# Kernel tuning notes

Measured on AMD Instinct MI355X. Metric: run time of the kernel, lower is better.

The kernel has to match this reference:

```python
import jax, jax.numpy as jnp
import numpy as np

B = 128        # graphs
NPG = 64       # nodes per graph (num_node)
N = B * NPG    # total nodes = 8192
IN = 16        # in_channels
D = 128        # d_model
OUT = 64       # out_channels
CAT = IN * NPG + NPG * NPG  # 5120
EPS = 1e-5


def _lin_init(k, fi, fo):
    s = 1.0 / np.sqrt(fi)
    kw, kb = jax.random.split(k)
    W = jax.random.uniform(kw, (fi, fo), jnp.float32, -s, s)
    b = jax.random.uniform(kb, (fo,), jnp.float32, -s, s)
    return W, b


def setup_inputs() -> dict:
    key = jax.random.key(0)
    ks = jax.random.split(key, 10)
    x = jax.random.normal(ks[0], (N, IN), jnp.float32)
    # complete graph (all i->j pairs, incl. self loops) per graph, offset per graph
    ii = np.repeat(np.arange(NPG), NPG)
    jj = np.tile(np.arange(NPG), NPG)
    off = (np.arange(B) * NPG)[:, None]
    row = (ii[None, :] + off).reshape(-1)
    col = (jj[None, :] + off).reshape(-1)
    edge_index = jnp.asarray(np.stack([row, col]), jnp.int32)  # [2, E]
    E = edge_index.shape[1]
    edge_weight = jax.random.uniform(ks[1], (E,), jnp.float32)
    batch = jnp.repeat(jnp.arange(B, dtype=jnp.int32), NPG)
    W1, b1 = _lin_init(ks[2], IN, D)
    W2, b2 = _lin_init(ks[3], D, D)
    Wm0, bm0 = _lin_init(ks[4], D + CAT, D)
    Wm1, bm1 = _lin_init(ks[5], D, D)
    Wm2, bm2 = _lin_init(ks[6], D, D)
    Wout, bout = _lin_init(ks[7], D, OUT)
    ones = jnp.ones((D,), jnp.float32)
    zeros = jnp.zeros((D,), jnp.float32)
    return dict(x=x, edge_index=edge_index, edge_weight=edge_weight, batch=batch,
                W1=W1, b1=b1, W2=W2, b2=b2,
                Wm0=Wm0, bm0=bm0, g0=ones, be0=zeros,
                Wm1=Wm1, bm1=bm1, g1=ones, be1=zeros,
                Wm2=Wm2, bm2=bm2, g2=ones, be2=zeros,
                Wout=Wout, bout=bout)


def _gcn_conv(h_in, row, col, ew, W, b):
    # PyG GCNConv: linear first, then D^-1/2 (A) D^-1/2 aggregation (self loops already present)
    h = h_in @ W                                             # [N, F]
    deg = jax.ops.segment_sum(ew, col, num_segments=N)       # in-degree by edge weight
    dinv = jnp.where(deg > 0, jax.lax.rsqrt(deg), 0.0)
    norm = dinv[row] * ew * dinv[col]                        # [E]
    out = jax.ops.segment_sum(norm[:, None] * h[row], col, num_segments=N)
    return out + b


def _bn(h, g, b):
    # BatchNorm1d, training-mode math (biased variance), eps=1e-5
    m = jnp.mean(h, axis=0)
    v = jnp.var(h, axis=0)
    return g * (h - m) * jax.lax.rsqrt(v + EPS) + b


def reference(x, edge_index, edge_weight, batch,
              W1, b1, W2, b2,
              Wm0, bm0, g0, be0,
              Wm1, bm1, g1, be1,
              Wm2, bm2, g2, be2,
              Wout, bout):
    row, col = edge_index[0], edge_index[1]
    h = _gcn_conv(x, row, col, edge_weight, W1, b1)
    h = jax.nn.relu(h)
    h = _gcn_conv(h, row, col, edge_weight, W2, b2)
    # global_mean_pool
    sums = jax.ops.segment_sum(h, batch, num_segments=B)
    cnt = jax.ops.segment_sum(jnp.ones((N,), h.dtype), batch, num_segments=B)
    pooled = sums / cnt[:, None]
    pooled = jax.nn.relu(pooled)
    feat = jnp.concatenate([pooled, x.reshape(B, -1), edge_weight.reshape(B, -1)], axis=1)
    feat = jax.nn.relu(feat)
    h = _bn(jax.nn.relu(feat @ Wm0 + bm0), g0, be0)
    h = _bn(jax.nn.relu(h @ Wm1 + bm1), g1, be1)
    h = _bn(jax.nn.relu(h @ Wm2 + bm2), g2, be2)
    return h @ Wout + bout
```

## Files before the change

### kernel.cpp

```cpp
#include <hip/hip_runtime.h>

#define NG 128
#define NPG 64
#define IN 16
#define DM 128
#define NOUT 64
#define EPG 4096
#define NCH 128
#define BN_EPS 1e-5f

__global__ __launch_bounds__(512) void k_front(
    const float* __restrict__ x, const float* __restrict__ ew,
    const float* __restrict__ W1, const float* __restrict__ b1,
    const float* __restrict__ W2, const float* __restrict__ b2,
    const float* __restrict__ Wm0,
    float* __restrict__ part, float* __restrict__ ppart,
    float* __restrict__ stats)
{
    __shared__ __align__(16) float u[16128];
    const int bid = blockIdx.x, t = threadIdx.x;

    if (bid < 128) {
        float* ew_s     = u;
        float* x_s      = u + 4096;
        float* W1_s     = u + 5120;
        float* P_s      = u + 7168;
        float* b1_s     = u + 15360;
        float* dinv_s   = u + 15488;
        float* t_s      = u + 15552;
        float* zp       = u + 4096;
        float* z_full   = u + 15616;
        float* pooled_s = u + 15744;
        float* pp4      = u + 4096;
        const int g = bid;
        if (bid == 0) {
            for (int i = t; i < 768; i += 512) stats[i] = 0.f;
        }
        {
            const float4* ew4 = (const float4*)(ew + g * EPG);
            float4* ews4 = (float4*)ew_s;
            ews4[t]       = ew4[t];
            ews4[t + 512] = ew4[t + 512];
            if (t < 256) {
                const int xi = t & 63, k4 = (t >> 6) * 4;
                float4 xv = *(const float4*)(x + g * NPG * IN + xi * IN + k4);
                x_s[(k4 + 0) * 64 + xi] = xv.x;
                x_s[(k4 + 1) * 64 + xi] = xv.y;
                x_s[(k4 + 2) * 64 + xi] = xv.z;
                x_s[(k4 + 3) * 64 + xi] = xv.w;
            }
            ((float4*)W1_s)[t] = ((const float4*)W1)[t];
            if (t < 128) b1_s[t] = b1[t];
        }
        __syncthreads();

        if (t < NPG) {
            float s = 0.f;
            #pragma unroll 8
            for (int i = 0; i < NPG; i++) s += ew_s[i * NPG + t];
            dinv_s[t] = (s > 0.f) ? rsqrtf(s) : 0.f;
        }
        __syncthreads();

        {
            const int j = t & 63, q = t >> 6;
            const float dj = dinv_s[j];
            for (int i = q * 8; i < q * 8 + 8; i++) {
                float vv = ew_s[i * NPG + j] * dj;
                #pragma unroll
                for (int off = 32; off > 0; off >>= 1) vv += __shfl_down(vv, off, 64);
                if (j == 0) t_s[i] = dinv_s[i] * vv * (1.f / 64.f);
            }
        }

        {
            const int it = t & 15, ft = t >> 4;
            const int i0 = it * 4, f0 = ft * 4;
            float accp[4][4];
            #pragma unroll
            for (int a = 0; a < 4; a++)
                #pragma unroll
                for (int c = 0; c < 4; c++) accp[a][c] = 0.f;
            #pragma unroll
            for (int k = 0; k < IN; k++) {
                const float4 a4 = *(const float4*)(x_s + k * 64 + i0);
                const float4 b4 = *(const float4*)(W1_s + k * DM + f0);
                const float av[4] = {a4.x, a4.y, a4.z, a4.w};
                const float bv[4] = {b4.x, b4.y, b4.z, b4.w};
                #pragma unroll
                for (int a = 0; a < 4; a++)
                    #pragma unroll
                    for (int c = 0; c < 4; c++) accp[a][c] += av[a] * bv[c];
            }
            #pragma unroll
            for (int a = 0; a < 4; a++) {
                const float di = dinv_s[i0 + a];
                *(float4*)(P_s + (i0 + a) * DM + f0) =
                    make_float4(di * accp[a][0], di * accp[a][1],
                                di * accp[a][2], di * accp[a][3]);
            }
        }
        __syncthreads();

        {
            const int jt = t & 15, ft = t >> 4;
            const int j0 = jt * 4, f0 = ft * 4;
            float acc[4][4];
            #pragma unroll
            for (int a = 0; a < 4; a++)
                #pragma unroll
                for (int c = 0; c < 4; c++) acc[a][c] = 0.f;
            #pragma unroll 4
            for (int k = 0; k < 64; k++) {
                const float4 a4 = *(const float4*)(ew_s + k * 64 + j0);
                const float4 b4 = *(const float4*)(P_s + k * DM + f0);
                const float av[4] = {a4.x, a4.y, a4.z, a4.w};
                const float bv[4] = {b4.x, b4.y, b4.z, b4.w};
                #pragma unroll
                for (int a = 0; a < 4; a++)
                    #pragma unroll
                    for (int c = 0; c < 4; c++) acc[a][c] += av[a] * bv[c];
            }
            float zpart[4];
            #pragma unroll
            for (int c = 0; c < 4; c++) zpart[c] = 0.f;
            #pragma unroll
            for (int a = 0; a < 4; a++) {
                const float dj = dinv_s[j0 + a], tj = t_s[j0 + a];
                #pragma unroll
                for (int c = 0; c < 4; c++) {
                    float h = fmaxf(dj * acc[a][c] + b1_s[f0 + c], 0.f);
                    zpart[c] += tj * h;
                }
            }
            *(float4*)(zp + jt * 132 + f0) =
                make_float4(zpart[0], zpart[1], zpart[2], zpart[3]);
        }
        __syncthreads();

        if (t < 128) {
            float s = 0.f;
            #pragma unroll
            for (int jt = 0; jt < 16; jt++) s += zp[jt * 132 + t];
            z_full[t] = s;
        }
        __syncthreads();

        {
            const int c = t & 127, kh = t >> 7;
            float acc = 0.f;
            #pragma unroll 8
            for (int k = kh * 32; k < kh * 32 + 32; k++)
                acc += z_full[k] * W2[k * DM + c];
            pp4[kh * 128 + c] = acc;
        }
        __syncthreads();
        if (t < 128)
            pooled_s[t] = fmaxf(pp4[t] + pp4[128 + t] + pp4[256 + t] + pp4[384 + t]
                                + b2[t], 0.f);
        __syncthreads();

        {
            const int f = t & 127, kh = t >> 7;
            float acc = 0.f;
            #pragma unroll 8
            for (int k = kh * 32; k < kh * 32 + 32; k++)
                acc += pooled_s[k] * Wm0[k * DM + f];
            pp4[kh * 128 + f] = acc;
        }
        __syncthreads();
        if (t < 128)
            ppart[g * DM + t] = pp4[t] + pp4[128 + t] + pp4[256 + t] + pp4[384 + t];
    } else {
        const int c = bid - 128;
        const int kc = c >> 1, fh = c & 1;
        const int K0 = kc * 80;
        float* a_s = u;
        float* b_s = u + 10560;

        float4 ra[4], ra2, rb[3];
        #pragma unroll
        for (int it = 0; it < 4; it++) {
            int idx = it * 512 + t;
            int gg = idx >> 4, k4 = (idx & 15) << 2;
            int K = K0 + k4;
            const float* src = (K < 1024) ? (x + gg * 1024 + K)
                                          : (ew + gg * 4096 + (K - 1024));
            ra[it] = *(const float4*)src;
        }
        {
            int gg = t >> 2, k4 = 64 + ((t & 3) << 2);
            int K = K0 + k4;
            const float* src = (K < 1024) ? (x + gg * 1024 + K)
                                          : (ew + gg * 4096 + (K - 1024));
            ra2 = *(const float4*)src;
        }
        #pragma unroll
        for (int it = 0; it < 3; it++) {
            int idx = it * 512 + t;
            if (idx < 1280) {
                int k = idx >> 4, fl4 = (idx & 15) << 2;
                rb[it] = *(const float4*)(Wm0 + (size_t)(128 + K0 + k) * 128
                                          + fh * 64 + fl4);
            }
        }
        #pragma unroll
        for (int it = 0; it < 4; it++) {
            int idx = it * 512 + t;
            int gg = idx >> 4, k4 = (idx & 15) << 2;
            a_s[(k4 + 0) * 132 + gg] = fmaxf(ra[it].x, 0.f);
            a_s[(k4 + 1) * 132 + gg] = fmaxf(ra[it].y, 0.f);
            a_s[(k4 + 2) * 132 + gg] = fmaxf(ra[it].z, 0.f);
            a_s[(k4 + 3) * 132 + gg] = fmaxf(ra[it].w, 0.f);
        }
        {
            int gg = t >> 2, k4 = 64 + ((t & 3) << 2);
            a_s[(k4 + 0) * 132 + gg] = fmaxf(ra2.x, 0.f);
            a_s[(k4 + 1) * 132 + gg] = fmaxf(ra2.y, 0.f);
            a_s[(k4 + 2) * 132 + gg] = fmaxf(ra2.z, 0.f);
            a_s[(k4 + 3) * 132 + gg] = fmaxf(ra2.w, 0.f);
        }
        #pragma unroll
        for (int it = 0; it < 3; it++) {
            int idx = it * 512 + t;
            if (idx < 1280) {
                int k = idx >> 4, fl4 = (idx & 15) << 2;
                *(float4*)(b_s + k * 64 + fl4) = rb[it];
            }
        }
        __syncthreads();

        const int gthr = t & 31, fthr = t >> 5;
        const int g0 = gthr * 4, f0 = fthr * 4;
        float acc[4][4];
        #pragma unroll
        for (int i = 0; i < 4; i++)
            #pragma unroll
            for (int jx = 0; jx < 4; jx++) acc[i][jx] = 0.f;

        #pragma unroll 4
        for (int k = 0; k < 80; k++) {
            const float4 a4 = *(const float4*)(a_s + k * 132 + g0);
            const float4 b4 = *(const float4*)(b_s + k * 64 + f0);
            const float av[4] = {a4.x, a4.y, a4.z, a4.w};
            const float bv[4] = {b4.x, b4.y, b4.z, b4.w};
            #pragma unroll
            for (int i = 0; i < 4; i++)
                #pragma unroll
                for (int jx = 0; jx < 4; jx++) acc[i][jx] += av[i] * bv[jx];
        }

        float* pp = part + (size_t)c * 8192;
        #pragma unroll
        for (int i = 0; i < 4; i++)
            *(float4*)(pp + (g0 + i) * 64 + f0) =
                make_float4(acc[i][0], acc[i][1], acc[i][2], acc[i][3]);
    }
}

__global__ __launch_bounds__(256) void k_reduce_bn0(
    const float* __restrict__ part, const float* __restrict__ ppart,
    const float* __restrict__ bm0, float* __restrict__ v0,
    float* __restrict__ stats0)
{
    __shared__ float r1[1024];
    __shared__ float sv[64], sv2[64];
    const int bx = blockIdx.x, t = threadIdx.x;
    const int fgrp = bx & 7, gt = bx >> 3;
    const int f4 = t & 3, gl = (t >> 2) & 3, ch = t >> 4;
    const int g = gt * 4 + gl;
    const int fbase = fgrp * 16 + f4 * 4;
    const int fh = fbase >> 6, fl = fbase & 63;

    const float4* p = (const float4*)part
                    + ((size_t)(2 * (ch * 4) + fh) * 8192 + g * 64 + fl) / 4;
    float4 v = make_float4(0.f, 0.f, 0.f, 0.f);
    #pragma unroll
    for (int cc = 0; cc < 4; cc++) {
        float4 x4 = p[(size_t)cc * 4096];
        v.x += x4.x; v.y += x4.y; v.z += x4.z; v.w += x4.w;
    }
    float* r = r1 + ch * 64 + gl * 16 + f4 * 4;
    r[0] = v.x; r[1] = v.y; r[2] = v.z; r[3] = v.w;
    __syncthreads();

    if (t < 64) {
        const int fsub = t & 15, gl2 = t >> 4;
        const int f = fgrp * 16 + fsub, gg = gt * 4 + gl2;
        float s = bm0[f] + ppart[gg * DM + f];
        #pragma unroll
        for (int c2 = 0; c2 < 16; c2++) s += r1[c2 * 64 + gl2 * 16 + fsub];
        s = fmaxf(s, 0.f);
        v0[gg * DM + f] = s;
        sv[t] = s; sv2[t] = s * s;
    }
    __syncthreads();
    if (t < 16) {
        float s1 = sv[t] + sv[t + 16] + sv[t + 32] + sv[t + 48];
        float s2 = sv2[t] + sv2[t + 16] + sv2[t + 32] + sv2[t + 48];
        atomicAdd(&stats0[(fgrp * 16 + t) * 2], s1);
        atomicAdd(&stats0[(fgrp * 16 + t) * 2 + 1], s2);
    }
}

__global__ __launch_bounds__(256) void k_mlp(
    const float* __restrict__ vin, const float* __restrict__ statsin,
    const float* __restrict__ gbn, const float* __restrict__ bbn,
    const float* __restrict__ W, const float* __restrict__ bias,
    float* __restrict__ vout, float* __restrict__ statsout)
{
    __shared__ float scale_s[128], shift_s[128];
    __shared__ float wcol[128];
    __shared__ float pc[256];
    __shared__ float h_s[64 * 129];
    const int b = blockIdx.x, t = threadIdx.x;
    const int f = b & 127, gh = b >> 7;
    if (t < 128) {
        float s1 = statsin[t * 2], s2 = statsin[t * 2 + 1];
        float m = s1 * (1.f / 128.f);
        float var = s2 * (1.f / 128.f) - m * m;
        float sc = gbn[t] * rsqrtf(var + BN_EPS);
        scale_s[t] = sc;
        shift_s[t] = bbn[t] - m * sc;
        wcol[t] = W[t * 128 + f];
    }
    __syncthreads();
    const int g0r = gh * 64;
    const float4* vin4 = (const float4*)(vin + g0r * 128);
    #pragma unroll
    for (int it = 0; it < 8; ++it) {
        int idx = it * 256 + t;
        int gl = idx >> 5, k4 = (idx & 31) * 4;
        float4 vv = vin4[idx];
        float* hp = h_s + gl * 129 + k4;
        hp[0] = vv.x * scale_s[k4 + 0] + shift_s[k4 + 0];
        hp[1] = vv.y * scale_s[k4 + 1] + shift_s[k4 + 1];
        hp[2] = vv.z * scale_s[k4 + 2] + shift_s[k4 + 2];
        hp[3] = vv.w * scale_s[k4 + 3] + shift_s[k4 + 3];
    }
    __syncthreads();
    {
        const int gl = t & 63, kh = t >> 6;
        float acc = 0.f;
        #pragma unroll 8
        for (int k = kh * 32; k < kh * 32 + 32; ++k) acc += h_s[gl * 129 + k] * wcol[k];
        pc[gl * 4 + kh] = acc;
    }
    __syncthreads();
    if (t < 64) {
        float v = fmaxf(pc[t * 4] + pc[t * 4 + 1] + pc[t * 4 + 2] + pc[t * 4 + 3]
                        + bias[f], 0.f);
        vout[(size_t)(g0r + t) * 128 + f] = v;
        float s1 = v, s2 = v * v;
        #pragma unroll
        for (int off = 32; off > 0; off >>= 1) {
            s1 += __shfl_down(s1, off, 64);
            s2 += __shfl_down(s2, off, 64);
        }
        if (t == 0) {
            atomicAdd(&statsout[f * 2], s1);
            atomicAdd(&statsout[f * 2 + 1], s2);
        }
    }
}

__global__ __launch_bounds__(128) void k_out(
    const float* __restrict__ vin, const float* __restrict__ statsin,
    const float* __restrict__ gbn, const float* __restrict__ bbn,
    const float* __restrict__ Wo, const float* __restrict__ bo,
    float* __restrict__ out)
{
    __shared__ __align__(16) float Wo_s[128 * 64];
    __shared__ float vrow[2][128];
    __shared__ float scale_s[128], shift_s[128];
    const int b = blockIdx.x, t = threadIdx.x, g0 = b * 2;
    {
        float s1 = statsin[t * 2], s2 = statsin[t * 2 + 1];
        float m = s1 * (1.f / 128.f);
        float var = s2 * (1.f / 128.f) - m * m;
        float sc = gbn[t] * rsqrtf(var + BN_EPS);
        scale_s[t] = sc;
        shift_s[t] = bbn[t] - m * sc;
    }
    __syncthreads();
    {
        const float4* wo4 = (const float4*)Wo;
        float4* wos4 = (float4*)Wo_s;
        #pragma unroll
        for (int it = 0; it < 16; it++) wos4[it * 128 + t] = wo4[it * 128 + t];
    }
    if (t < 64) {
        int g2 = t >> 5, k4 = (t & 31) * 4;
        float4 vv = ((const float4*)(vin + g0 * 128))[t];
        vrow[g2][k4 + 0] = vv.x * scale_s[k4 + 0] + shift_s[k4 + 0];
        vrow[g2][k4 + 1] = vv.y * scale_s[k4 + 1] + shift_s[k4 + 1];
        vrow[g2][k4 + 2] = vv.z * scale_s[k4 + 2] + shift_s[k4 + 2];
        vrow[g2][k4 + 3] = vv.w * scale_s[k4 + 3] + shift_s[k4 + 3];
    }
    __syncthreads();
    const int g2 = t >> 6, o = t & 63;
    float acc = bo[o];
    #pragma unroll 8
    for (int k = 0; k < 128; k++) acc += vrow[g2][k] * Wo_s[k * 64 + o];
    out[(g0 + g2) * NOUT + o] = acc;
}

extern "C" void kernel_launch(void* const* d_in, const int* in_sizes, int n_in,
                              void* d_out, int out_size, void* d_ws, size_t ws_size,
                              hipStream_t stream)
{
    const float* x   = (const float*)d_in[0];
    const float* ew  = (const float*)d_in[2];
    const float* W1  = (const float*)d_in[4];
    const float* b1  = (const float*)d_in[5];
    const float* W2  = (const float*)d_in[6];
    const float* b2  = (const float*)d_in[7];
    const float* Wm0 = (const float*)d_in[8];
    const float* bm0 = (const float*)d_in[9];
    const float* g0  = (const float*)d_in[10];
    const float* be0 = (const float*)d_in[11];
    const float* Wm1 = (const float*)d_in[12];
    const float* bm1 = (const float*)d_in[13];
    const float* g1  = (const float*)d_in[14];
    const float* be1 = (const float*)d_in[15];
    const float* Wm2 = (const float*)d_in[16];
    const float* bm2 = (const float*)d_in[17];
    const float* g2  = (const float*)d_in[18];
    const float* be2 = (const float*)d_in[19];
    const float* Wo  = (const float*)d_in[20];
    const float* bo  = (const float*)d_in[21];

    float* ws     = (float*)d_ws;
    float* part   = ws;
    float* ppartb = part + NCH * 8192;
    float* v0     = ppartb + 16384;
    float* v1     = v0 + 16384;
    float* v2     = v1 + 16384;
    float* stats  = v2 + 16384;

    k_front<<<256, 512, 0, stream>>>(x, ew, W1, b1, W2, b2, Wm0, part, ppartb, stats);
    k_reduce_bn0<<<256, 256, 0, stream>>>(part, ppartb, bm0, v0, stats);
    k_mlp<<<256, 256, 0, stream>>>(v0, stats,       g0, be0, Wm1, bm1, v1, stats + 256);
    k_mlp<<<256, 256, 0, stream>>>(v1, stats + 256, g1, be1, Wm2, bm2, v2, stats + 512);
    k_out<<<NOUT, 128, 0, stream>>>(v2, stats + 512, g2, be2, Wo, bo, (float*)d_out);
}
```

Baseline: 132.5 us.

## Fuse reduce, MLP layers and output into one persistent kernel with grid barriers

Replaces the four tail launches (the partial-sum reduce with BN0 stats, two MLP layers, and the output projection) with a single 256-block kernel. The phases are separated by a hierarchical atomic grid barrier whose counters and flags live in a memset-cleared region of the workspace. Stores that cross phases use agent-scope atomic stores, and each waiting block issues an acquire fence after the barrier. This removes per-launch overhead and inter-kernel gaps. In exchange it adds a memset node, relies on all 256 blocks being co-resident, and spins on barrier flags.

```diff
diff --git a/kernel.cpp b/kernel.cpp
--- a/kernel.cpp
+++ b/kernel.cpp
@@ -8,6 +8,32 @@
 #define EPG 4096
 #define NCH 128
 #define BN_EPS 1e-5f
+
+__device__ __forceinline__ void stg(float* p, float v) {
+    __hip_atomic_store(p, v, __ATOMIC_RELAXED, __HIP_MEMORY_SCOPE_AGENT);
+}
+
+__device__ __forceinline__ void gbar(unsigned* bu, unsigned e, int bid, int t,
+                                     bool wait) {
+    __syncthreads();
+    if (t == 0) {
+        unsigned* sub   = bu + e * 160 + (bid & 7) * 16;
+        unsigned* root  = bu + e * 160 + 128;
+        unsigned* flags = bu + 1024;
+        if (atomicAdd(sub, 1u) == 31u)
+            if (atomicAdd(root, 1u) == 7u)
+                for (int i = 0; i < 256; i++)
+                    __hip_atomic_store(&flags[i * 16], e,
+                                       __ATOMIC_RELAXED, __HIP_MEMORY_SCOPE_AGENT);
+        if (wait) {
+            while (__hip_atomic_load(&flags[bid * 16],
+                                     __ATOMIC_RELAXED, __HIP_MEMORY_SCOPE_AGENT) < e)
+                __builtin_amdgcn_s_sleep(1);
+            __builtin_amdgcn_fence(__ATOMIC_ACQUIRE, "agent");
+        }
+    }
+    __syncthreads();
+}
 
 __global__ __launch_bounds__(512) void k_front(
     const float* __restrict__ x, const float* __restrict__ ew,
@@ -258,63 +284,18 @@
     }
 }
 
-__global__ __launch_bounds__(256) void k_reduce_bn0(
-    const float* __restrict__ part, const float* __restrict__ ppart,
-    const float* __restrict__ bm0, float* __restrict__ v0,
-    float* __restrict__ stats0)
-{
-    __shared__ float r1[1024];
-    __shared__ float sv[64], sv2[64];
-    const int bx = blockIdx.x, t = threadIdx.x;
-    const int fgrp = bx & 7, gt = bx >> 3;
-    const int f4 = t & 3, gl = (t >> 2) & 3, ch = t >> 4;
-    const int g = gt * 4 + gl;
-    const int fbase = fgrp * 16 + f4 * 4;
-    const int fh = fbase >> 6, fl = fbase & 63;
-
-    const float4* p = (const float4*)part
-                    + ((size_t)(2 * (ch * 4) + fh) * 8192 + g * 64 + fl) / 4;
-    float4 v = make_float4(0.f, 0.f, 0.f, 0.f);
-    #pragma unroll
-    for (int cc = 0; cc < 4; cc++) {
-        float4 x4 = p[(size_t)cc * 4096];
-        v.x += x4.x; v.y += x4.y; v.z += x4.z; v.w += x4.w;
-    }
-    float* r = r1 + ch * 64 + gl * 16 + f4 * 4;
-    r[0] = v.x; r[1] = v.y; r[2] = v.z; r[3] = v.w;
-    __syncthreads();
-
-    if (t < 64) {
-        const int fsub = t & 15, gl2 = t >> 4;
-        const int f = fgrp * 16 + fsub, gg = gt * 4 + gl2;
-        float s = bm0[f] + ppart[gg * DM + f];
-        #pragma unroll
-        for (int c2 = 0; c2 < 16; c2++) s += r1[c2 * 64 + gl2 * 16 + fsub];
-        s = fmaxf(s, 0.f);
-        v0[gg * DM + f] = s;
-        sv[t] = s; sv2[t] = s * s;
-    }
-    __syncthreads();
-    if (t < 16) {
-        float s1 = sv[t] + sv[t + 16] + sv[t + 32] + sv[t + 48];
-        float s2 = sv2[t] + sv2[t + 16] + sv2[t + 32] + sv2[t + 48];
-        atomicAdd(&stats0[(fgrp * 16 + t) * 2], s1);
-        atomicAdd(&stats0[(fgrp * 16 + t) * 2 + 1], s2);
-    }
-}
-
-__global__ __launch_bounds__(256) void k_mlp(
+__device__ void mlp_phase(float* u, int bid, int t,
     const float* __restrict__ vin, const float* __restrict__ statsin,
     const float* __restrict__ gbn, const float* __restrict__ bbn,
     const float* __restrict__ W, const float* __restrict__ bias,
     float* __restrict__ vout, float* __restrict__ statsout)
 {
-    __shared__ float scale_s[128], shift_s[128];
-    __shared__ float wcol[128];
-    __shared__ float pc[256];
-    __shared__ float h_s[64 * 129];
-    const int b = blockIdx.x, t = threadIdx.x;
-    const int f = b & 127, gh = b >> 7;
+    float* scale_s = u;
+    float* shift_s = u + 128;
+    float* wcol    = u + 256;
+    float* pc      = u + 384;
+    float* h_s     = u + 640;
+    const int f = bid & 127, gh = bid >> 7;
     if (t < 128) {
         float s1 = statsin[t * 2], s2 = statsin[t * 2 + 1];
         float m = s1 * (1.f / 128.f);
@@ -343,14 +324,15 @@
         const int gl = t & 63, kh = t >> 6;
         float acc = 0.f;
         #pragma unroll 8
-        for (int k = kh * 32; k < kh * 32 + 32; ++k) acc += h_s[gl * 129 + k] * wcol[k];
+        for (int k = kh * 32; k < kh * 32 + 32; ++k)
+            acc += h_s[gl * 129 + k] * wcol[k];
         pc[gl * 4 + kh] = acc;
     }
     __syncthreads();
     if (t < 64) {
         float v = fmaxf(pc[t * 4] + pc[t * 4 + 1] + pc[t * 4 + 2] + pc[t * 4 + 3]
                         + bias[f], 0.f);
-        vout[(size_t)(g0r + t) * 128 + f] = v;
+        stg(&vout[(size_t)(g0r + t) * 128 + f], v);
         float s1 = v, s2 = v * v;
         #pragma unroll
         for (int off = 32; off > 0; off >>= 1) {
@@ -364,45 +346,109 @@
     }
 }
 
-__global__ __launch_bounds__(128) void k_out(
-    const float* __restrict__ vin, const float* __restrict__ statsin,
-    const float* __restrict__ gbn, const float* __restrict__ bbn,
+__global__ __launch_bounds__(256) void k_tail(
+    const float* __restrict__ part, const float* __restrict__ ppart,
+    const float* __restrict__ bm0,
+    const float* __restrict__ gbn0, const float* __restrict__ bbn0,
+    const float* __restrict__ Wm1, const float* __restrict__ bm1,
+    const float* __restrict__ gbn1, const float* __restrict__ bbn1,
+    const float* __restrict__ Wm2, const float* __restrict__ bm2,
+    const float* __restrict__ gbn2, const float* __restrict__ bbn2,
     const float* __restrict__ Wo, const float* __restrict__ bo,
-    float* __restrict__ out)
+    float* __restrict__ ws, float* __restrict__ out)
 {
-    __shared__ __align__(16) float Wo_s[128 * 64];
-    __shared__ float vrow[2][128];
-    __shared__ float scale_s[128], shift_s[128];
-    const int b = blockIdx.x, t = threadIdx.x, g0 = b * 2;
+    __shared__ __align__(16) float u[9216];
+    unsigned* bu = (unsigned*)ws;
+    float* stats = ws + 1292288;
+    float* v0    = ws + 1243136;
+    float* v1    = v0 + 16384;
+    float* v2    = v1 + 16384;
+    const int bid = blockIdx.x, t = threadIdx.x;
+
     {
-        float s1 = statsin[t * 2], s2 = statsin[t * 2 + 1];
-        float m = s1 * (1.f / 128.f);
-        float var = s2 * (1.f / 128.f) - m * m;
-        float sc = gbn[t] * rsqrtf(var + BN_EPS);
-        scale_s[t] = sc;
-        shift_s[t] = bbn[t] - m * sc;
-    }
-    __syncthreads();
+        float* r1  = u;
+        float* sv  = u + 1024;
+        float* sv2 = u + 1088;
+        const int fgrp = bid & 7, gt = bid >> 3;
+        const int f4 = t & 3, gl = (t >> 2) & 3, ch = t >> 4;
+        const int g = gt * 4 + gl;
+        const int fbase = fgrp * 16 + f4 * 4;
+        const int fh = fbase >> 6, fl = fbase & 63;
+        const float4* p = (const float4*)part
+                        + ((size_t)(2 * (ch * 4) + fh) * 8192 + g * 64 + fl) / 4;
+        float4 v = make_float4(0.f, 0.f, 0.f, 0.f);
+        #pragma unroll
+        for (int cc = 0; cc < 4; cc++) {
+            float4 x4 = p[(size_t)cc * 4096];
+            v.x += x4.x; v.y += x4.y; v.z += x4.z; v.w += x4.w;
+        }
+        float* r = r1 + ch * 64 + gl * 16 + f4 * 4;
+        r[0] = v.x; r[1] = v.y; r[2] = v.z; r[3] = v.w;
+        __syncthreads();
+
+        if (t < 64) {
+            const int fsub = t & 15, gl2 = t >> 4;
+            const int f = fgrp * 16 + fsub, gg = gt * 4 + gl2;
+            float s = bm0[f] + ppart[gg * DM + f];
+            #pragma unroll
+            for (int c2 = 0; c2 < 16; c2++) s += r1[c2 * 64 + gl2 * 16 + fsub];
+            s = fmaxf(s, 0.f);
+            stg(&v0[gg * DM + f], s);
+            sv[t] = s; sv2[t] = s * s;
+        }
+        __syncthreads();
+        if (t < 16) {
+            float s1 = sv[t] + sv[t + 16] + sv[t + 32] + sv[t + 48];
+            float s2 = sv2[t] + sv2[t + 16] + sv2[t + 32] + sv2[t + 48];
+            atomicAdd(&stats[(fgrp * 16 + t) * 2], s1);
+            atomicAdd(&stats[(fgrp * 16 + t) * 2 + 1], s2);
+        }
+    }
+    gbar(bu, 1u, bid, t, true);
+
+    mlp_phase(u, bid, t, v0, stats,       gbn0, bbn0, Wm1, bm1, v1, stats + 256);
+    gbar(bu, 2u, bid, t, true);
+    mlp_phase(u, bid, t, v1, stats + 256, gbn1, bbn1, Wm2, bm2, v2, stats + 512);
+    gbar(bu, 3u, bid, t, bid < 128);
+    if (bid >= 128) return;
+
     {
-        const float4* wo4 = (const float4*)Wo;
-        float4* wos4 = (float4*)Wo_s;
-        #pragma unroll
-        for (int it = 0; it < 16; it++) wos4[it * 128 + t] = wo4[it * 128 + t];
-    }
-    if (t < 64) {
-        int g2 = t >> 5, k4 = (t & 31) * 4;
-        float4 vv = ((const float4*)(vin + g0 * 128))[t];
-        vrow[g2][k4 + 0] = vv.x * scale_s[k4 + 0] + shift_s[k4 + 0];
-        vrow[g2][k4 + 1] = vv.y * scale_s[k4 + 1] + shift_s[k4 + 1];
-        vrow[g2][k4 + 2] = vv.z * scale_s[k4 + 2] + shift_s[k4 + 2];
-        vrow[g2][k4 + 3] = vv.w * scale_s[k4 + 3] + shift_s[k4 + 3];
-    }
-    __syncthreads();
-    const int g2 = t >> 6, o = t & 63;
-    float acc = bo[o];
-    #pragma unroll 8
-    for (int k = 0; k < 128; k++) acc += vrow[g2][k] * Wo_s[k * 64 + o];
-    out[(g0 + g2) * NOUT + o] = acc;
+        float* Wo_s = u;
+        float* vrow = u + 8192;
+        float* sc   = u + 8320;
+        float* sh   = u + 8448;
+        float* pc   = u + 8576;
+        const float* st2 = stats + 512;
+        const int g = bid;
+        if (t < 128) {
+            float s1 = st2[t * 2], s2 = st2[t * 2 + 1];
+            float m = s1 * (1.f / 128.f);
+            float var = s2 * (1.f / 128.f) - m * m;
+            float scv = gbn2[t] * rsqrtf(var + BN_EPS);
+            sc[t] = scv;
+            sh[t] = bbn2[t] - m * scv;
+        }
+        {
+            const float4* wo4 = (const float4*)Wo;
+            float4* wos4 = (float4*)Wo_s;
+            #pragma unroll
+            for (int it = 0; it < 8; it++) wos4[it * 256 + t] = wo4[it * 256 + t];
+        }
+        __syncthreads();
+        if (t < 128) vrow[t] = v2[(size_t)g * 128 + t] * sc[t] + sh[t];
+        __syncthreads();
+        {
+            const int o = t & 63, kh = t >> 6;
+            float acc = 0.f;
+            #pragma unroll 8
+            for (int k = kh * 32; k < kh * 32 + 32; k++)
+                acc += vrow[k] * Wo_s[k * 64 + o];
+            pc[kh * 64 + o] = acc;
+        }
+        __syncthreads();
+        if (t < 64)
+            out[g * NOUT + t] = pc[t] + pc[64 + t] + pc[128 + t] + pc[192 + t] + bo[t];
+    }
 }
 
 extern "C" void kernel_launch(void* const* d_in, const int* in_sizes, int n_in,
@@ -431,16 +477,20 @@
     const float* bo  = (const float*)d_in[21];
 
     float* ws     = (float*)d_ws;
-    float* part   = ws;
+    float* part   = ws + 5120;
     float* ppartb = part + NCH * 8192;
     float* v0     = ppartb + 16384;
+    v0 = ws + 1243136;
     float* v1     = v0 + 16384;
     float* v2     = v1 + 16384;
-    float* stats  = v2 + 16384;
-
-    k_front<<<256, 512, 0, stream>>>(x, ew, W1, b1, W2, b2, Wm0, part, ppartb, stats);
-    k_reduce_bn0<<<256, 256, 0, stream>>>(part, ppartb, bm0, v0, stats);
-    k_mlp<<<256, 256, 0, stream>>>(v0, stats,       g0, be0, Wm1, bm1, v1, stats + 256);
-    k_mlp<<<256, 256, 0, stream>>>(v1, stats + 256, g1, be1, Wm2, bm2, v2, stats + 512);
-    k_out<<<NOUT, 128, 0, stream>>>(v2, stats + 512, g2, be2, Wo, bo, (float*)d_out);
-}
+    float* stats  = ws + 1292288;
+
+    hipMemsetAsync(d_ws, 0, 20480, stream);
+    k_front<<<256, 512, 0, stream>>>(x, ew, W1, b1, W2, b2, Wm0,
+                                     part, ppartb, stats);
+    k_tail<<<256, 256, 0, stream>>>(part, ppartb, bm0,
+                                    g0, be0, Wm1, bm1,
+                                    g1, be1, Wm2, bm2,
+                                    g2, be2, Wo, bo,
+                                    ws, (float*)d_out);
+}
```

New measurement: 134.3 us. Within noise of the previous version (+1.3%).

## Fuse MLP tail into one kernel and rework split-K GEMM tiling

Applied to the files above, without the earlier changes.

The big concat GEMM is repartitioned: 32 blocks each cover a 32-graph by 64-feature tile over a 1280-wide K chunk. Each block double-buffers its shared-memory tiles with register prefetch and splits K across four thread groups, reducing them in shared memory. The split-K reduction, three BN/MLP layers and the output linear are fused into one tail kernel, launched as 64 redundant blocks that each recompute the whole 128x128 MLP. This cuts five launches to two and drops the stats atomics and workspace round-trips, at the cost of redundant per-block work and fewer blocks on the GEMM.

```diff
diff --git a/kernel.cpp b/kernel.cpp
--- a/kernel.cpp
+++ b/kernel.cpp
@@ -1,21 +1,19 @@
 #include <hip/hip_runtime.h>
 
-#define NG 128
 #define NPG 64
 #define IN 16
 #define DM 128
 #define NOUT 64
 #define EPG 4096
-#define NCH 128
 #define BN_EPS 1e-5f
+
 
 __global__ __launch_bounds__(512) void k_front(
     const float* __restrict__ x, const float* __restrict__ ew,
     const float* __restrict__ W1, const float* __restrict__ b1,
     const float* __restrict__ W2, const float* __restrict__ b2,
     const float* __restrict__ Wm0,
-    float* __restrict__ part, float* __restrict__ ppart,
-    float* __restrict__ stats)
+    float* __restrict__ part, float* __restrict__ ppart)
 {
     __shared__ __align__(16) float u[16128];
     const int bid = blockIdx.x, t = threadIdx.x;
@@ -33,9 +31,6 @@
         float* pooled_s = u + 15744;
         float* pp4      = u + 4096;
         const int g = bid;
-        if (bid == 0) {
-            for (int i = t; i < 768; i += 512) stats[i] = 0.f;
-        }
         {
             const float4* ew4 = (const float4*)(ew + g * EPG);
             float4* ews4 = (float4*)ew_s;
@@ -173,236 +168,262 @@
             ppart[g * DM + t] = pp4[t] + pp4[128 + t] + pp4[256 + t] + pp4[384 + t];
     } else {
         const int c = bid - 128;
-        const int kc = c >> 1, fh = c & 1;
-        const int K0 = kc * 80;
+        const int gt = c & 3, ftb = (c >> 2) & 1, kc = c >> 3;
+        const int gB = gt * 32, fB = ftb * 64, K0 = kc * 1280;
         float* a_s = u;
-        float* b_s = u + 10560;
-
-        float4 ra[4], ra2, rb[3];
-        #pragma unroll
-        for (int it = 0; it < 4; it++) {
-            int idx = it * 512 + t;
-            int gg = idx >> 4, k4 = (idx & 15) << 2;
-            int K = K0 + k4;
-            const float* src = (K < 1024) ? (x + gg * 1024 + K)
-                                          : (ew + gg * 4096 + (K - 1024));
-            ra[it] = *(const float4*)src;
-        }
-        {
-            int gg = t >> 2, k4 = 64 + ((t & 3) << 2);
-            int K = K0 + k4;
-            const float* src = (K < 1024) ? (x + gg * 1024 + K)
-                                          : (ew + gg * 4096 + (K - 1024));
-            ra2 = *(const float4*)src;
-        }
-        #pragma unroll
-        for (int it = 0; it < 3; it++) {
-            int idx = it * 512 + t;
-            if (idx < 1280) {
-                int k = idx >> 4, fl4 = (idx & 15) << 2;
-                rb[it] = *(const float4*)(Wm0 + (size_t)(128 + K0 + k) * 128
-                                          + fh * 64 + fl4);
-            }
-        }
-        #pragma unroll
-        for (int it = 0; it < 4; it++) {
-            int idx = it * 512 + t;
-            int gg = idx >> 4, k4 = (idx & 15) << 2;
-            a_s[(k4 + 0) * 132 + gg] = fmaxf(ra[it].x, 0.f);
-            a_s[(k4 + 1) * 132 + gg] = fmaxf(ra[it].y, 0.f);
-            a_s[(k4 + 2) * 132 + gg] = fmaxf(ra[it].z, 0.f);
-            a_s[(k4 + 3) * 132 + gg] = fmaxf(ra[it].w, 0.f);
-        }
-        {
-            int gg = t >> 2, k4 = 64 + ((t & 3) << 2);
-            a_s[(k4 + 0) * 132 + gg] = fmaxf(ra2.x, 0.f);
-            a_s[(k4 + 1) * 132 + gg] = fmaxf(ra2.y, 0.f);
-            a_s[(k4 + 2) * 132 + gg] = fmaxf(ra2.z, 0.f);
-            a_s[(k4 + 3) * 132 + gg] = fmaxf(ra2.w, 0.f);
-        }
-        #pragma unroll
-        for (int it = 0; it < 3; it++) {
-            int idx = it * 512 + t;
-            if (idx < 1280) {
-                int k = idx >> 4, fl4 = (idx & 15) << 2;
-                *(float4*)(b_s + k * 64 + fl4) = rb[it];
-            }
-        }
-        __syncthreads();
-
-        const int gthr = t & 31, fthr = t >> 5;
-        const int g0 = gthr * 4, f0 = fthr * 4;
+        float* b_s = u + 4608;
+
+        const int kq = t >> 7;
+        const int id = t & 127;
+        const int g0 = (id & 7) * 4;
+        const int f0 = (id >> 3) * 4;
+        const int sgg = t & 31;
+        const int skk = (t >> 5) * 4;
+
         float acc[4][4];
         #pragma unroll
         for (int i = 0; i < 4; i++)
             #pragma unroll
-            for (int jx = 0; jx < 4; jx++) acc[i][jx] = 0.f;
-
-        #pragma unroll 4
-        for (int k = 0; k < 80; k++) {
-            const float4 a4 = *(const float4*)(a_s + k * 132 + g0);
-            const float4 b4 = *(const float4*)(b_s + k * 64 + f0);
-            const float av[4] = {a4.x, a4.y, a4.z, a4.w};
-            const float bv[4] = {b4.x, b4.y, b4.z, b4.w};
+            for (int j = 0; j < 4; j++) acc[i][j] = 0.f;
+
+        float4 rA, rB0, rB1;
+        auto LOADF = [&](int ci) {
+            int K = K0 + ci * 64 + skk;
+            const float* src = (K < 1024) ? (x + (size_t)(gB + sgg) * 1024 + K)
+                                          : (ew + (size_t)(gB + sgg) * 4096 + (K - 1024));
+            rA = *(const float4*)src;
+            int kk0 = t >> 4, ff0 = (t & 15) * 4;
+            rB0 = *(const float4*)(Wm0 + (size_t)(128 + K0 + ci * 64 + kk0) * 128
+                                   + fB + ff0);
+            int kk1 = 32 + (t >> 4);
+            rB1 = *(const float4*)(Wm0 + (size_t)(128 + K0 + ci * 64 + kk1) * 128
+                                   + fB + ff0);
+        };
+        auto STOREF = [&](int buf) {
+            float* ab = a_s + buf * 2304;
+            ab[(skk + 0) * 36 + sgg] = fmaxf(rA.x, 0.f);
+            ab[(skk + 1) * 36 + sgg] = fmaxf(rA.y, 0.f);
+            ab[(skk + 2) * 36 + sgg] = fmaxf(rA.z, 0.f);
+            ab[(skk + 3) * 36 + sgg] = fmaxf(rA.w, 0.f);
+            float* bb = b_s + buf * 4352;
+            int kk0 = t >> 4, ff0 = (t & 15) * 4;
+            *(float4*)(bb + kk0 * 68 + ff0) = rB0;
+            *(float4*)(bb + (32 + kk0) * 68 + ff0) = rB1;
+        };
+        auto COMPF = [&](int buf) {
+            const float* ab = a_s + buf * 2304;
+            const float* bb = b_s + buf * 4352;
+            #pragma unroll 4
+            for (int k2 = 0; k2 < 16; k2++) {
+                const int k = kq * 16 + k2;
+                const float4 a = *(const float4*)(ab + k * 36 + g0);
+                const float4 b = *(const float4*)(bb + k * 68 + f0);
+                const float av[4] = {a.x, a.y, a.z, a.w};
+                const float bv[4] = {b.x, b.y, b.z, b.w};
+                #pragma unroll
+                for (int i = 0; i < 4; i++)
+                    #pragma unroll
+                    for (int j = 0; j < 4; j++) acc[i][j] += av[i] * bv[j];
+            }
+        };
+
+        LOADF(0); STOREF(0);
+        __syncthreads();
+        for (int ci = 0; ci < 20; ci++) {
+            if (ci < 19) LOADF(ci + 1);
+            COMPF(ci & 1);
+            if (ci < 19) STOREF((ci + 1) & 1);
+            __syncthreads();
+        }
+        float* red = u;
+        if (kq > 0) {
+            float* r = red + (kq - 1) * 2048 + id * 16;
             #pragma unroll
             for (int i = 0; i < 4; i++)
                 #pragma unroll
-                for (int jx = 0; jx < 4; jx++) acc[i][jx] += av[i] * bv[jx];
-        }
-
-        float* pp = part + (size_t)c * 8192;
+                for (int j = 0; j < 4; j++) r[i * 4 + j] = acc[i][j];
+        }
+        __syncthreads();
+        if (kq == 0) {
+            #pragma unroll
+            for (int i = 0; i < 4; i++)
+                #pragma unroll
+                for (int j = 0; j < 4; j++)
+                    acc[i][j] += red[id * 16 + i * 4 + j]
+                               + red[2048 + id * 16 + i * 4 + j]
+                               + red[4096 + id * 16 + i * 4 + j];
+            #pragma unroll
+            for (int i = 0; i < 4; i++)
+                *(float4*)(part + (size_t)kc * 16384
+                           + (size_t)(gB + g0 + i) * 128 + fB + f0) =
+                    make_float4(acc[i][0], acc[i][1], acc[i][2], acc[i][3]);
+        }
+    }
+}
+
+__device__ __forceinline__ void mlayer(
+    float* ht, float* sp1, float* sp2, float* scs, float* shs, int t,
+    const float* __restrict__ W, const float* __restrict__ bias,
+    const float* __restrict__ gbn, const float* __restrict__ bbn)
+{
+    const int gthr = t & 31, f0 = (t >> 5) * 8;
+    const int g0 = gthr * 4;
+    float acc[4][8];
+    #pragma unroll
+    for (int i = 0; i < 4; i++)
+        #pragma unroll
+        for (int j = 0; j < 8; j++) acc[i][j] = 0.f;
+    #pragma unroll 2
+    for (int k = 0; k < 128; k++) {
+        const float4 a  = *(const float4*)(ht + k * 128 + g0);
+        const float4 w0 = *(const float4*)(W + (size_t)k * 128 + f0);
+        const float4 w1 = *(const float4*)(W + (size_t)k * 128 + f0 + 4);
+        const float av[4] = {a.x, a.y, a.z, a.w};
+        const float wv[8] = {w0.x, w0.y, w0.z, w0.w, w1.x, w1.y, w1.z, w1.w};
         #pragma unroll
         for (int i = 0; i < 4; i++)
-            *(float4*)(pp + (g0 + i) * 64 + f0) =
-                make_float4(acc[i][0], acc[i][1], acc[i][2], acc[i][3]);
-    }
+            #pragma unroll
+            for (int j = 0; j < 8; j++) acc[i][j] += av[i] * wv[j];
+    }
+    const float4 bA = *(const float4*)(bias + f0);
+    const float4 bB = *(const float4*)(bias + f0 + 4);
+    const float bv[8] = {bA.x, bA.y, bA.z, bA.w, bB.x, bB.y, bB.z, bB.w};
+    float v[4][8];
+    #pragma unroll
+    for (int i = 0; i < 4; i++)
+        #pragma unroll
+        for (int j = 0; j < 8; j++) v[i][j] = fmaxf(acc[i][j] + bv[j], 0.f);
+    float p1[8], p2[8];
+    #pragma unroll
+    for (int j = 0; j < 8; j++) {
+        p1[j] = v[0][j] + v[1][j] + v[2][j] + v[3][j];
+        p2[j] = v[0][j] * v[0][j] + v[1][j] * v[1][j]
+              + v[2][j] * v[2][j] + v[3][j] * v[3][j];
+    }
+    #pragma unroll
+    for (int off = 16; off > 0; off >>= 1)
+        #pragma unroll
+        for (int j = 0; j < 8; j++) {
+            p1[j] += __shfl_xor(p1[j], off, 64);
+            p2[j] += __shfl_xor(p2[j], off, 64);
+        }
+    if (gthr == 0)
+        #pragma unroll
+        for (int j = 0; j < 8; j++) { sp1[f0 + j] = p1[j]; sp2[f0 + j] = p2[j]; }
+    __syncthreads();
+    if (t < 128) {
+        float m = sp1[t] * (1.f / 128.f);
+        float var = sp2[t] * (1.f / 128.f) - m * m;
+        float s = gbn[t] * rsqrtf(var + BN_EPS);
+        scs[t] = s; shs[t] = bbn[t] - m * s;
+    }
+    __syncthreads();
+    #pragma unroll
+    for (int j = 0; j < 8; j++) {
+        const float sj = scs[f0 + j], hj = shs[f0 + j];
+        *(float4*)(ht + (f0 + j) * 128 + g0) =
+            make_float4(v[0][j] * sj + hj, v[1][j] * sj + hj,
+                        v[2][j] * sj + hj, v[3][j] * sj + hj);
+    }
+    __syncthreads();
 }
 
-__global__ __launch_bounds__(256) void k_reduce_bn0(
+__global__ __launch_bounds__(512) void k_tail(
     const float* __restrict__ part, const float* __restrict__ ppart,
-    const float* __restrict__ bm0, float* __restrict__ v0,
-    float* __restrict__ stats0)
-{
-    __shared__ float r1[1024];
-    __shared__ float sv[64], sv2[64];
-    const int bx = blockIdx.x, t = threadIdx.x;
-    const int fgrp = bx & 7, gt = bx >> 3;
-    const int f4 = t & 3, gl = (t >> 2) & 3, ch = t >> 4;
-    const int g = gt * 4 + gl;
-    const int fbase = fgrp * 16 + f4 * 4;
-    const int fh = fbase >> 6, fl = fbase & 63;
-
-    const float4* p = (const float4*)part
-                    + ((size_t)(2 * (ch * 4) + fh) * 8192 + g * 64 + fl) / 4;
-    float4 v = make_float4(0.f, 0.f, 0.f, 0.f);
-    #pragma unroll
-    for (int cc = 0; cc < 4; cc++) {
-        float4 x4 = p[(size_t)cc * 4096];
-        v.x += x4.x; v.y += x4.y; v.z += x4.z; v.w += x4.w;
-    }
-    float* r = r1 + ch * 64 + gl * 16 + f4 * 4;
-    r[0] = v.x; r[1] = v.y; r[2] = v.z; r[3] = v.w;
-    __syncthreads();
-
-    if (t < 64) {
-        const int fsub = t & 15, gl2 = t >> 4;
-        const int f = fgrp * 16 + fsub, gg = gt * 4 + gl2;
-        float s = bm0[f] + ppart[gg * DM + f];
-        #pragma unroll
-        for (int c2 = 0; c2 < 16; c2++) s += r1[c2 * 64 + gl2 * 16 + fsub];
-        s = fmaxf(s, 0.f);
-        v0[gg * DM + f] = s;
-        sv[t] = s; sv2[t] = s * s;
-    }
-    __syncthreads();
-    if (t < 16) {
-        float s1 = sv[t] + sv[t + 16] + sv[t + 32] + sv[t + 48];
-        float s2 = sv2[t] + sv2[t + 16] + sv2[t + 32] + sv2[t + 48];
-        atomicAdd(&stats0[(fgrp * 16 + t) * 2], s1);
-        atomicAdd(&stats0[(fgrp * 16 + t) * 2 + 1], s2);
-    }
-}
-
-__global__ __launch_bounds__(256) void k_mlp(
-    const float* __restrict__ vin, const float* __restrict__ statsin,
-    const float* __restrict__ gbn, const float* __restrict__ bbn,
-    const float* __restrict__ W, const float* __restrict__ bias,
-    float* __restrict__ vout, float* __restrict__ statsout)
-{
-    __shared__ float scale_s[128], shift_s[128];
-    __shared__ float wcol[128];
-    __shared__ float pc[256];
-    __shared__ float h_s[64 * 129];
-    const int b = blockIdx.x, t = threadIdx.x;
-    const int f = b & 127, gh = b >> 7;
-    if (t < 128) {
-        float s1 = statsin[t * 2], s2 = statsin[t * 2 + 1];
-        float m = s1 * (1.f / 128.f);
-        float var = s2 * (1.f / 128.f) - m * m;
-        float sc = gbn[t] * rsqrtf(var + BN_EPS);
-        scale_s[t] = sc;
-        shift_s[t] = bbn[t] - m * sc;
-        wcol[t] = W[t * 128 + f];
-    }
-    __syncthreads();
-    const int g0r = gh * 64;
-    const float4* vin4 = (const float4*)(vin + g0r * 128);
-    #pragma unroll
-    for (int it = 0; it < 8; ++it) {
-        int idx = it * 256 + t;
-        int gl = idx >> 5, k4 = (idx & 31) * 4;
-        float4 vv = vin4[idx];
-        float* hp = h_s + gl * 129 + k4;
-        hp[0] = vv.x * scale_s[k4 + 0] + shift_s[k4 + 0];
-        hp[1] = vv.y * scale_s[k4 + 1] + shift_s[k4 + 1];
-        hp[2] = vv.z * scale_s[k4 + 2] + shift_s[k4 + 2];
-        hp[3] = vv.w * scale_s[k4 + 3] + shift_s[k4 + 3];
-    }
-    __syncthreads();
-    {
-        const int gl = t & 63, kh = t >> 6;
-        float acc = 0.f;
-        #pragma unroll 8
-        for (int k = kh * 32; k < kh * 32 + 32; ++k) acc += h_s[gl * 129 + k] * wcol[k];
-        pc[gl * 4 + kh] = acc;
-    }
-    __syncthreads();
-    if (t < 64) {
-        float v = fmaxf(pc[t * 4] + pc[t * 4 + 1] + pc[t * 4 + 2] + pc[t * 4 + 3]
-                        + bias[f], 0.f);
-        vout[(size_t)(g0r + t) * 128 + f] = v;
-        float s1 = v, s2 = v * v;
-        #pragma unroll
-        for (int off = 32; off > 0; off >>= 1) {
-            s1 += __shfl_down(s1, off, 64);
-            s2 += __shfl_down(s2, off, 64);
-        }
-        if (t == 0) {
-            atomicAdd(&statsout[f * 2], s1);
-            atomicAdd(&statsout[f * 2 + 1], s2);
-        }
-    }
-}
-
-__global__ __launch_bounds__(128) void k_out(
-    const float* __restrict__ vin, const float* __restrict__ statsin,
-    const float* __restrict__ gbn, const float* __restrict__ bbn,
+    const float* __restrict__ bm0,
+    const float* __restrict__ gbn0, const float* __restrict__ bbn0,
+    const float* __restrict__ Wm1, const float* __restrict__ bm1,
+    const float* __restrict__ gbn1, const float* __restrict__ bbn1,
+    const float* __restrict__ Wm2, const float* __restrict__ bm2,
+    const float* __restrict__ gbn2, const float* __restrict__ bbn2,
     const float* __restrict__ Wo, const float* __restrict__ bo,
     float* __restrict__ out)
 {
-    __shared__ __align__(16) float Wo_s[128 * 64];
-    __shared__ float vrow[2][128];
-    __shared__ float scale_s[128], shift_s[128];
-    const int b = blockIdx.x, t = threadIdx.x, g0 = b * 2;
+    __shared__ __align__(16) float ht[128 * 128];
+    __shared__ float sp1[128], sp2[128], scs[128], shs[128];
+    const int bid = blockIdx.x, t = threadIdx.x;
+    const int gthr = t & 31, f0 = (t >> 5) * 8;
+    const int g0 = gthr * 4;
+
+    float vr[4][8];
     {
-        float s1 = statsin[t * 2], s2 = statsin[t * 2 + 1];
-        float m = s1 * (1.f / 128.f);
-        float var = s2 * (1.f / 128.f) - m * m;
-        float sc = gbn[t] * rsqrtf(var + BN_EPS);
-        scale_s[t] = sc;
-        shift_s[t] = bbn[t] - m * sc;
-    }
-    __syncthreads();
+        const float4 bA = *(const float4*)(bm0 + f0);
+        const float4 bB = *(const float4*)(bm0 + f0 + 4);
+        #pragma unroll
+        for (int i = 0; i < 4; i++) {
+            const size_t ro = (size_t)(g0 + i) * 128 + f0;
+            float4 sA = *(const float4*)(ppart + ro);
+            float4 sB = *(const float4*)(ppart + ro + 4);
+            sA.x += bA.x; sA.y += bA.y; sA.z += bA.z; sA.w += bA.w;
+            sB.x += bB.x; sB.y += bB.y; sB.z += bB.z; sB.w += bB.w;
+            #pragma unroll
+            for (int kc = 0; kc < 4; kc++) {
+                float4 pA = *(const float4*)(part + kc * 16384 + ro);
+                float4 pB = *(const float4*)(part + kc * 16384 + ro + 4);
+                sA.x += pA.x; sA.y += pA.y; sA.z += pA.z; sA.w += pA.w;
+                sB.x += pB.x; sB.y += pB.y; sB.z += pB.z; sB.w += pB.w;
+            }
+            vr[i][0] = fmaxf(sA.x, 0.f); vr[i][1] = fmaxf(sA.y, 0.f);
+            vr[i][2] = fmaxf(sA.z, 0.f); vr[i][3] = fmaxf(sA.w, 0.f);
+            vr[i][4] = fmaxf(sB.x, 0.f); vr[i][5] = fmaxf(sB.y, 0.f);
+            vr[i][6] = fmaxf(sB.z, 0.f); vr[i][7] = fmaxf(sB.w, 0.f);
+        }
+    }
     {
-        const float4* wo4 = (const float4*)Wo;
-        float4* wos4 = (float4*)Wo_s;
-        #pragma unroll
-        for (int it = 0; it < 16; it++) wos4[it * 128 + t] = wo4[it * 128 + t];
-    }
-    if (t < 64) {
-        int g2 = t >> 5, k4 = (t & 31) * 4;
-        float4 vv = ((const float4*)(vin + g0 * 128))[t];
-        vrow[g2][k4 + 0] = vv.x * scale_s[k4 + 0] + shift_s[k4 + 0];
-        vrow[g2][k4 + 1] = vv.y * scale_s[k4 + 1] + shift_s[k4 + 1];
-        vrow[g2][k4 + 2] = vv.z * scale_s[k4 + 2] + shift_s[k4 + 2];
-        vrow[g2][k4 + 3] = vv.w * scale_s[k4 + 3] + shift_s[k4 + 3];
-    }
-    __syncthreads();
-    const int g2 = t >> 6, o = t & 63;
-    float acc = bo[o];
-    #pragma unroll 8
-    for (int k = 0; k < 128; k++) acc += vrow[g2][k] * Wo_s[k * 64 + o];
-    out[(g0 + g2) * NOUT + o] = acc;
+        float p1[8], p2[8];
+        #pragma unroll
+        for (int j = 0; j < 8; j++) {
+            p1[j] = vr[0][j] + vr[1][j] + vr[2][j] + vr[3][j];
+            p2[j] = vr[0][j] * vr[0][j] + vr[1][j] * vr[1][j]
+                  + vr[2][j] * vr[2][j] + vr[3][j] * vr[3][j];
+        }
+        #pragma unroll
+        for (int off = 16; off > 0; off >>= 1)
+            #pragma unroll
+            for (int j = 0; j < 8; j++) {
+                p1[j] += __shfl_xor(p1[j], off, 64);
+                p2[j] += __shfl_xor(p2[j], off, 64);
+            }
+        if (gthr == 0)
+            #pragma unroll
+            for (int j = 0; j < 8; j++) { sp1[f0 + j] = p1[j]; sp2[f0 + j] = p2[j]; }
+    }
+    #pragma unroll
+    for (int j = 0; j < 8; j++)
+        *(float4*)(ht + (f0 + j) * 128 + g0) =
+            make_float4(vr[0][j], vr[1][j], vr[2][j], vr[3][j]);
+    __syncthreads();
+    if (t < 128) {
+        float m = sp1[t] * (1.f / 128.f);
+        float var = sp2[t] * (1.f / 128.f) - m * m;
+        float s = gbn0[t] * rsqrtf(var + BN_EPS);
+        scs[t] = s; shs[t] = bbn0[t] - m * s;
+    }
+    __syncthreads();
+    {
+        const int k = t >> 2, sg = (t & 3) * 32;
+        const float sck = scs[k], shk = shs[k];
+        float4* hp = (float4*)(ht + k * 128 + sg);
+        #pragma unroll
+        for (int q = 0; q < 8; q++) {
+            float4 v2 = hp[q];
+            hp[q] = make_float4(v2.x * sck + shk, v2.y * sck + shk,
+                                v2.z * sck + shk, v2.w * sck + shk);
+        }
+    }
+    __syncthreads();
+
+    mlayer(ht, sp1, sp2, scs, shs, t, Wm1, bm1, gbn1, bbn1);
+    mlayer(ht, sp1, sp2, scs, shs, t, Wm2, bm2, gbn2, bbn2);
+
+    if (t < 128) {
+        const int gs = t >> 6, o = t & 63;
+        const int gg = bid * 2 + gs;
+        float a = bo[o];
+        #pragma unroll 8
+        for (int k = 0; k < 128; k++) a += ht[k * 128 + gg] * Wo[k * 64 + o];
+        out[gg * NOUT + o] = a;
+    }
 }
 
 extern "C" void kernel_launch(void* const* d_in, const int* in_sizes, int n_in,
@@ -430,17 +451,14 @@
     const float* Wo  = (const float*)d_in[20];
     const float* bo  = (const float*)d_in[21];
 
-    float* ws     = (float*)d_ws;
-    float* part   = ws;
-    float* ppartb = part + NCH * 8192;
-    float* v0     = ppartb + 16384;
-    float* v1     = v0 + 16384;
-    float* v2     = v1 + 16384;
-    float* stats  = v2 + 16384;
-
-    k_front<<<256, 512, 0, stream>>>(x, ew, W1, b1, W2, b2, Wm0, part, ppartb, stats);
-    k_reduce_bn0<<<256, 256, 0, stream>>>(part, ppartb, bm0, v0, stats);
-    k_mlp<<<256, 256, 0, stream>>>(v0, stats,       g0, be0, Wm1, bm1, v1, stats + 256);
-    k_mlp<<<256, 256, 0, stream>>>(v1, stats + 256, g1, be1, Wm2, bm2, v2, stats + 512);
-    k_out<<<NOUT, 128, 0, stream>>>(v2, stats + 512, g2, be2, Wo, bo, (float*)d_out);
+    float* ws    = (float*)d_ws;
+    float* part  = ws;
+    float* ppart = ws + 65536;
+
+    k_front<<<160, 512, 0, stream>>>(x, ew, W1, b1, W2, b2, Wm0, part, ppart);
+    k_tail<<<64, 512, 0, stream>>>(part, ppart, bm0,
+                                   g0, be0, Wm1, bm1,
+                                   g1, be1, Wm2, bm2,
+                                   g2, be2, Wo, bo,
+                                   (float*)d_out);
 }
```

New measurement: 185.6 us. +40.1%, slower.
